# Kernel tuning notes

Hardware: AMD Instinct MI355X
Metric: run time of the kernel (lower is better)

## Reference

```python
import jax, jax.numpy as jnp
import numpy as np

N = 100000
INPLANES = 256
WIDTH = 104          # floor(256 * 26 / 64)
SCALE = 4
NUMS = SCALE - 1     # 3 branch convs
K = 27               # 3^3 kernel offsets for 3D kernel_size=3
EPS = 1e-5


def setup_inputs() -> dict:
    key = jax.random.key(0)
    ks = jax.random.split(key, 12)
    x_feat = jax.random.normal(ks[0], (N, INPLANES), dtype=jnp.float32)
    # neighbor map: index N means "no neighbor" (padded zero row)
    nbr_idx = jax.random.randint(ks[1], (N, K), 0, N + 1)
    ws = WIDTH * SCALE
    W1 = jax.random.normal(ks[2], (INPLANES, ws), dtype=jnp.float32) * (1.0 / np.sqrt(INPLANES))
    g1 = jnp.ones((ws,), jnp.float32)
    b1 = jnp.zeros((ws,), jnp.float32)
    Wc = jax.random.normal(ks[3], (NUMS, K, WIDTH, WIDTH), dtype=jnp.float32) * (1.0 / np.sqrt(K * WIDTH))
    gc = jnp.ones((NUMS, WIDTH), jnp.float32)
    bc = jnp.zeros((NUMS, WIDTH), jnp.float32)
    W3 = jax.random.normal(ks[4], (ws, INPLANES), dtype=jnp.float32) * (1.0 / np.sqrt(ws))
    g3 = jnp.ones((INPLANES,), jnp.float32)
    b3 = jnp.zeros((INPLANES,), jnp.float32)
    return {"x_feat": x_feat, "nbr_idx": nbr_idx, "W1": W1, "g1": g1, "b1": b1,
            "Wc": Wc, "gc": gc, "bc": bc, "W3": W3, "g3": g3, "b3": b3}


def _bn(x, g, b):
    # training-mode batch norm over the point dimension
    m = jnp.mean(x, axis=0)
    v = jnp.var(x, axis=0)
    return (x - m) * jax.lax.rsqrt(v + EPS) * g + b


def _sparse_conv(feat, nbr_idx, Wk):
    # gather-GEMM-scatter sparse conv: out[n] = sum_k feat[nbr[n,k]] @ Wk[k]
    # index == N hits the appended zero row (missing neighbor)
    fp = jnp.concatenate([feat, jnp.zeros((1, feat.shape[1]), feat.dtype)], axis=0)
    out = jnp.zeros((feat.shape[0], Wk.shape[2]), feat.dtype)
    for k in range(Wk.shape[0]):  # fixed small set of 27 kernel offsets
        out = out + fp[nbr_idx[:, k]] @ Wk[k]
    return out


def reference(x_feat, nbr_idx, W1, g1, b1, Wc, gc, bc, W3, g3, b3):
    out = jax.nn.relu(_bn(x_feat @ W1, g1, b1))          # [N, width*scale]
    spx = [out[:, i * WIDTH:(i + 1) * WIDTH] for i in range(SCALE)]
    parts = []
    sp = None
    for i in range(NUMS):
        # stype='normal', same coord map -> features_at_coordinates is identity
        sp_in = spx[i] if i == 0 else sp + spx[i]
        sp = jax.nn.relu(_bn(_sparse_conv(sp_in, nbr_idx, Wc[i]), gc[i], bc[i]))
        parts.append(sp)
    parts.append(spx[SCALE - 1])                          # scale != 1, normal
    cat = jnp.concatenate(parts, axis=1)                  # [N, width*scale]
    out = _bn(cat @ W3, g3, b3) + x_feat                  # residual (no downsample)
    return jax.nn.relu(out)
```

## Files before the change

kernel.cpp:

```cpp
#include <hip/hip_runtime.h>

#define NPTS 100000
#define INC 256
#define WID 104
#define WSC 416
#define KOFF 27
#define EPSV 1e-5f

typedef unsigned short u16;
typedef float f32x4 __attribute__((ext_vector_type(4)));
typedef short s16x8 __attribute__((ext_vector_type(8)));

__device__ __forceinline__ u16 f2bf(float f) {
  unsigned u = __builtin_bit_cast(unsigned, f);
  u += 0x7FFFu + ((u >> 16) & 1u);
  return (u16)(u >> 16);
}
__device__ __forceinline__ float bf2f(u16 h) {
  unsigned u = ((unsigned)h) << 16;
  return __builtin_bit_cast(float, u);
}
__device__ __forceinline__ void mfma16(f32x4& d, s16x8 a, s16x8 b) {
  asm("v_mfma_f32_16x16x32_bf16 %0, %1, %2, %0" : "+v"(d) : "v"(a), "v"(b));
}
__device__ __forceinline__ void rawbar() {
  __builtin_amdgcn_s_barrier();
  __builtin_amdgcn_sched_barrier(0);
}

#define ST1_OFF 0
#define STC_OFF 6656
#define STC_SZ 1664
#define ST3_OFF 11648
#define ST_TOTAL 15744

#define SPAD 128

__global__ __launch_bounds__(256) void k_prep_w1w3(const float* __restrict__ w1,
    const float* __restrict__ w3, u16* __restrict__ w1t, u16* __restrict__ w3t) {
  int i = blockIdx.x * 256 + threadIdx.x;
  if (i < 416 * 256) {
    int n = i >> 8, k = i & 255;
    w1t[i] = f2bf(w1[(size_t)k * WSC + n]);
  } else if (i < 2 * 416 * 256) {
    int o = i - 416 * 256;
    int n = o / WSC, k = o - n * WSC;
    w3t[o] = f2bf(w3[(size_t)k * INC + n]);
  }
}

__global__ __launch_bounds__(256) void k_prep_wc(const float* __restrict__ wc,
                                                 u16* __restrict__ wct) {
  __shared__ float w[WID * WID];
  int b = blockIdx.x, t = threadIdx.x;
  const float* s = wc + (size_t)b * WID * WID;
  for (int i = t; i < WID * WID; i += 256) w[i] = s[i];
  __syncthreads();
  u16* d = wct + (size_t)b * 112 * WID;
  for (int o = t; o < 112 * WID; o += 256) {
    int n = o / WID, kin = o - n * WID;
    d[o] = f2bf((n < WID) ? w[kin * WID + n] : 0.f);
  }
}

__global__ void k_init(float* __restrict__ st, u16* __restrict__ spxp) {
  const s16x8 hz = {0, 0, 0, 0, 0, 0, 0, 0};
  int i = blockIdx.x * 256 + threadIdx.x;
  if (i < ST_TOTAL) st[i] = 0.f;
  for (int task = i; task < (NPTS + 1) * 3; task += gridDim.x * 256) {
    int r = task / 3, c = task - 3 * r;
    *(s16x8*)(spxp + (size_t)r * SPAD + (13 + c) * 8) = hz;
  }
  if (blockIdx.x == 0 && threadIdx.x < 13)
    *(s16x8*)(spxp + (size_t)NPTS * SPAD + threadIdx.x * 8) = hz;
}

__global__ __launch_bounds__(256) void k_xbf(const float* __restrict__ x,
                                             u16* __restrict__ xb) {
  const int total = NPTS * INC / 8;
  for (int i = blockIdx.x * 256 + threadIdx.x; i < total; i += gridDim.x * 256) {
    const f32x4* s = (const f32x4*)(x + (size_t)i * 8);
    f32x4 v0 = s[0], v1 = s[1];
    s16x8 h;
#pragma unroll
    for (int j = 0; j < 4; ++j) { h[j] = (short)f2bf(v0[j]); h[4 + j] = (short)f2bf(v1[j]); }
    *(s16x8*)(xb + (size_t)i * 8) = h;
  }
}

__global__ __launch_bounds__(256) void k_gemm1(const u16* __restrict__ xb,
    const u16* __restrict__ w1t, u16* __restrict__ ys, float* __restrict__ stats) {
  const int n = blockIdx.x, xcd = n & 7, sgrp = n >> 3;
  const int cb = sgrp & 3, q = sgrp >> 2;
  const int rowbase = (xcd + 8 * q) * 128;
  if (rowbase >= NPTS) return;
  __shared__ char Al[128 * 128];
  __shared__ char Bl[112 * 128];
  const int t = threadIdx.x;
  const int lane = t & 63, wv = t >> 6, lr = lane & 15, lg = lane >> 4;
  const f32x4 fz = {0.f, 0.f, 0.f, 0.f};
  const s16x8 hz = {0, 0, 0, 0, 0, 0, 0, 0};
  f32x4 acc[2][7];
#pragma unroll
  for (int i = 0; i < 2; ++i)
#pragma unroll
    for (int j = 0; j < 7; ++j) acc[i][j] = fz;
  s16x8 pa[4], pb[4];

  auto issue = [&](int st) {
#pragma unroll
    for (int it = 0; it < 4; ++it) {
      int task = t + it * 256, r = task >> 3, c = task & 7, gr = rowbase + r;
      pa[it] = hz;
      if (gr < NPTS) pa[it] = *(const s16x8*)(xb + (size_t)gr * INC + st * 64 + c * 8);
      pb[it] = hz;
      if (task < 832)
        pb[it] = *(const s16x8*)(w1t + (size_t)(cb * WID + r) * INC + st * 64 + c * 8);
    }
  };
  auto writeT = [&]() {
#pragma unroll
    for (int it = 0; it < 4; ++it) {
      int task = t + it * 256, r = task >> 3, c = task & 7;
      *(s16x8*)(Al + ((r * 128 + c * 16) ^ ((r & 7) << 4))) = pa[it];
      if (task < 896) *(s16x8*)(Bl + ((r * 128 + c * 16) ^ ((r & 7) << 4))) = pb[it];
    }
  };
  auto compute = [&]() {
#pragma unroll
    for (int kc = 0; kc < 2; ++kc) {
      int co = kc * 64 + lg * 16;
      s16x8 a[2], b[7];
#pragma unroll
      for (int mt = 0; mt < 2; ++mt) {
        int r = wv * 32 + mt * 16 + lr;
        a[mt] = *(const s16x8*)(Al + ((r * 128 + co) ^ ((r & 7) << 4)));
      }
#pragma unroll
      for (int ct = 0; ct < 7; ++ct) {
        int r = ct * 16 + lr;
        b[ct] = *(const s16x8*)(Bl + ((r * 128 + co) ^ ((r & 7) << 4)));
      }
#pragma unroll
      for (int mt = 0; mt < 2; ++mt)
#pragma unroll
        for (int ct = 0; ct < 7; ++ct) mfma16(acc[mt][ct], a[mt], b[ct]);
    }
  };

  issue(0);
  for (int st = 0; st < 4; ++st) {
    writeT();
    __syncthreads();
    if (st < 3) issue(st + 1);
    compute();
    if (st < 3) rawbar();
  }
  __syncthreads();
  float* S = (float*)Al;
#pragma unroll
  for (int ct = 0; ct < 7; ++ct) {
    float s = 0.f, qq = 0.f;
#pragma unroll
    for (int mt = 0; mt < 2; ++mt)
#pragma unroll
      for (int j = 0; j < 4; ++j) { float v = acc[mt][ct][j]; s += v; qq += v * v; }
    s += __shfl_xor(s, 16); s += __shfl_xor(s, 32);
    qq += __shfl_xor(qq, 16); qq += __shfl_xor(qq, 32);
    if (lane < 16) {
      S[wv * 224 + ct * 16 + lane] = s;
      S[wv * 224 + 112 + ct * 16 + lane] = qq;
    }
  }
  __syncthreads();
  if (t < 224) {
    float v = S[t] + S[224 + t] + S[448 + t] + S[672 + t];
    int cl = (t < 112) ? t : t - 112;
    if (cl < WID) {
      float* base = stats + (sgrp & 7) * 832;
      atomicAdd(base + ((t < 112) ? 0 : WSC) + cb * WID + cl, v);
    }
  }
  __syncthreads();
#pragma unroll
  for (int mt = 0; mt < 2; ++mt)
#pragma unroll
    for (int ct = 0; ct < 7; ++ct)
#pragma unroll
      for (int j = 0; j < 4; ++j) {
        int r = rowbase + wv * 32 + mt * 16 + lg * 4 + j;
        int cl = ct * 16 + lr;
        if (r < NPTS && cl < WID)
          ys[((size_t)cb * NPTS + r) * WID + cl] = f2bf(acc[mt][ct][j]);
      }
}

__global__ __launch_bounds__(256) void k_conv(const u16* __restrict__ src,
    const int* __restrict__ nbr, const u16* __restrict__ wct,
    u16* __restrict__ z, float* __restrict__ stats) {
  __shared__ char Bl[112 * 208 + 64];
  const int t = threadIdx.x, rowbase = blockIdx.x * 128;
  const int lane = t & 63, wv = t >> 6, lr = lane & 15, lg = lane >> 4;
  const f32x4 fz = {0.f, 0.f, 0.f, 0.f};
  f32x4 acc[2][7];
#pragma unroll
  for (int i = 0; i < 2; ++i)
#pragma unroll
    for (int j = 0; j < 7; ++j) acc[i][j] = fz;
  s16x8 pa[2][4], pb[6];

  const int rm0 = rowbase + wv * 32 + lr, rm1 = rm0 + 16;
  const bool ok0 = rm0 < NPTS, ok1 = rm1 < NPTS;
  const int* np0 = nbr + (size_t)(ok0 ? rm0 : 0) * KOFF;
  const int* np1 = nbr + (size_t)(ok1 ? rm1 : 0) * KOFF;
  int in0, in1;

  auto loadB = [&](int k) {
#pragma unroll
    for (int it = 0; it < 6; ++it) {
      int task = t + it * 256;
      if (task < 1456) {
        int r = task / 13, c = task - 13 * r;
        pb[it] = *(const s16x8*)(wct + ((size_t)k * 112 + r) * WID + c * 8);
      }
    }
  };
  auto writeB = [&]() {
#pragma unroll
    for (int it = 0; it < 6; ++it) {
      int task = t + it * 256;
      if (task < 1456) {
        int r = task / 13, c = task - 13 * r;
        *(s16x8*)(Bl + r * 208 + c * 16) = pb[it];
      }
    }
  };

  {
    int i0 = ok0 ? np0[0] : NPTS, i1 = ok1 ? np1[0] : NPTS;
#pragma unroll
    for (int kc = 0; kc < 4; ++kc) {
      pa[0][kc] = *(const s16x8*)(src + (size_t)i0 * SPAD + kc * 32 + lg * 8);
      pa[1][kc] = *(const s16x8*)(src + (size_t)i1 * SPAD + kc * 32 + lg * 8);
    }
    loadB(0);
    in0 = ok0 ? np0[1] : NPTS;
    in1 = ok1 ? np1[1] : NPTS;
  }

  for (int k = 0; k < KOFF; ++k) {
    writeB();
    __syncthreads();
    if (k < KOFF - 1) loadB(k + 1);
    const bool more = k < KOFF - 1;
#pragma unroll
    for (int kc = 0; kc < 4; ++kc) {
      s16x8 bf[7];
#pragma unroll
      for (int ct = 0; ct < 7; ++ct)
        bf[ct] = *(const s16x8*)(Bl + (ct * 16 + lr) * 208 + kc * 64 + lg * 16);
#pragma unroll
      for (int ct = 0; ct < 7; ++ct) {
        mfma16(acc[0][ct], pa[0][kc], bf[ct]);
        mfma16(acc[1][ct], pa[1][kc], bf[ct]);
      }
      if (more) {
        pa[0][kc] = *(const s16x8*)(src + (size_t)in0 * SPAD + kc * 32 + lg * 8);
        pa[1][kc] = *(const s16x8*)(src + (size_t)in1 * SPAD + kc * 32 + lg * 8);
      }
    }
    if (k < KOFF - 2) {
      in0 = ok0 ? np0[k + 2] : NPTS;
      in1 = ok1 ? np1[k + 2] : NPTS;
    }
    rawbar();
  }

  __syncthreads();
  float* S = (float*)Bl;
#pragma unroll
  for (int ct = 0; ct < 7; ++ct) {
    float s = 0.f, qq = 0.f;
#pragma unroll
    for (int mt = 0; mt < 2; ++mt)
#pragma unroll
      for (int j = 0; j < 4; ++j) { float v = acc[mt][ct][j]; s += v; qq += v * v; }
    s += __shfl_xor(s, 16); s += __shfl_xor(s, 32);
    qq += __shfl_xor(qq, 16); qq += __shfl_xor(qq, 32);
    if (lane < 16) {
      S[wv * 224 + ct * 16 + lane] = s;
      S[wv * 224 + 112 + ct * 16 + lane] = qq;
    }
  }
  __syncthreads();
  if (t < 224) {
    float v = S[t] + S[224 + t] + S[448 + t] + S[672 + t];
    int cl = (t < 112) ? t : t - 112;
    if (cl < WID) {
      float* base = stats + (blockIdx.x & 7) * 208;
      atomicAdd(base + ((t < 112) ? 0 : WID) + cl, v);
    }
  }
#pragma unroll
  for (int mt = 0; mt < 2; ++mt)
#pragma unroll
    for (int ct = 0; ct < 7; ++ct)
#pragma unroll
      for (int j = 0; j < 4; ++j) {
        int r = rowbase + wv * 32 + mt * 16 + lg * 4 + j;
        int cl = ct * 16 + lr;
        if (r < NPTS && cl < WID)
          z[(size_t)r * WID + cl] = f2bf(acc[mt][ct][j]);
      }
}

__global__ __launch_bounds__(256) void k_gemm3(const u16* __restrict__ z0,
    const u16* __restrict__ z1, const u16* __restrict__ z2, const u16* __restrict__ ys,
    const u16* __restrict__ w3t, const float* __restrict__ ST,
    const float* __restrict__ gcp, const float* __restrict__ bcp,
    const float* __restrict__ g1, const float* __restrict__ b1,
    u16* __restrict__ ob, float* __restrict__ st3) {
  const int n = blockIdx.x, xcd = n & 7, sgrp = n >> 3;
  const int cb = sgrp & 1, q = sgrp >> 1;
  const int rowbase = (xcd + 8 * q) * 128;
  if (rowbase >= NPTS) return;
  __shared__ char Al[128 * 128];
  __shared__ char Bl[128 * 128];
  __shared__ float sscl[416], ssft[416];
  const int t = threadIdx.x;
  const int lane = t & 63, wv = t >> 6, lr = lane & 15, lg = lane >> 4;
  const int wr = wv >> 1, wc = wv & 1;
  const f32x4 fz = {0.f, 0.f, 0.f, 0.f};
  const s16x8 hz = {0, 0, 0, 0, 0, 0, 0, 0};
  const u16* ys3 = ys + (size_t)3 * NPTS * WID;
  for (int i = t; i < 416; i += 256) {
    float s = 0.f, qq = 0.f, gg, bb;
    if (i < 312) {
      int p = i / 104, c = i - p * 104;
      const float* base = ST + STC_OFF + p * STC_SZ;
#pragma unroll
      for (int bk = 0; bk < 8; ++bk) { s += base[bk * 208 + c]; qq += base[bk * 208 + 104 + c]; }
      gg = gcp[i]; bb = bcp[i];
    } else {
#pragma unroll
      for (int bk = 0; bk < 8; ++bk) { s += ST[bk * 832 + i]; qq += ST[bk * 832 + 416 + i]; }
      gg = g1[i]; bb = b1[i];
    }
    float m = s * (1.f / NPTS);
    float var = qq * (1.f / NPTS) - m * m;
    float rs = rsqrtf(var + EPSV);
    float sc = rs * gg;
    sscl[i] = sc; ssft[i] = bb - m * sc;
  }
  f32x4 acc[4][4];
#pragma unroll
  for (int i = 0; i < 4; ++i)
#pragma unroll
    for (int j = 0; j < 4; ++j) acc[i][j] = fz;
  s16x8 pa[4], pb[4];

  auto issue = [&](int st) {
#pragma unroll
    for (int it = 0; it < 4; ++it) {
      int task = t + it * 256, r = task >> 3, c = task & 7;
      int gr = rowbase + r, gq = st * 8 + c;
      pa[it] = hz;
      if (gr < NPTS && gq < 52) {
        int p = gq / 13, cc8 = (gq - p * 13) * 8;
        const u16* s = (p == 0) ? z0 + (size_t)gr * WID + cc8
                     : (p == 1) ? z1 + (size_t)gr * WID + cc8
                     : (p == 2) ? z2 + (size_t)gr * WID + cc8
                                : ys3 + (size_t)gr * WID + cc8;
        pa[it] = *(const s16x8*)s;
      }
      int gk = st * 64 + c * 8;
      pb[it] = hz;
      if (gk < WSC) pb[it] = *(const s16x8*)(w3t + (size_t)(cb * 128 + r) * WSC + gk);
    }
  };
  auto writeT = [&](int st) {
#pragma unroll
    for (int it = 0; it < 4; ++it) {
      int task = t + it * 256, r = task >> 3, c = task & 7;
      int gr = rowbase + r, gq = st * 8 + c;
      s16x8 h = hz;
      if (gr < NPTS && gq < 52) {
        int p = gq / 13;
        int colb = p * WID + (gq - p * 13) * 8;
#pragma unroll
        for (int j = 0; j < 8; ++j) {
          float f = fmaxf(bf2f((u16)pa[it][j]) * sscl[colb + j] + ssft[colb + j], 0.f);
          h[j] = (short)f2bf(f);
        }
      }
      *(s16x8*)(Al + ((r * 128 + c * 16) ^ ((r & 7) << 4))) = h;
      *(s16x8*)(Bl + ((r * 128 + c * 16) ^ ((r & 7) << 4))) = pb[it];
    }
  };
  auto compute = [&]() {
#pragma unroll
    for (int kc = 0; kc < 2; ++kc) {
      int co = kc * 64 + lg * 16;
      s16x8 a[4], b[4];
#pragma unroll
      for (int mt = 0; mt < 4; ++mt) {
        int r = wr * 64 + mt * 16 + lr;
        a[mt] = *(const s16x8*)(Al + ((r * 128 + co) ^ ((r & 7) << 4)));
      }
#pragma unroll
      for (int ct = 0; ct < 4; ++ct) {
        int r = wc * 64 + ct * 16 + lr;
        b[ct] = *(const s16x8*)(Bl + ((r * 128 + co) ^ ((r & 7) << 4)));
      }
#pragma unroll
      for (int mt = 0; mt < 4; ++mt)
#pragma unroll
        for (int ct = 0; ct < 4; ++ct) mfma16(acc[mt][ct], a[mt], b[ct]);
    }
  };

  issue(0);
  __syncthreads();
  for (int st = 0; st < 7; ++st) {
    writeT(st);
    __syncthreads();
    if (st < 6) issue(st + 1);
    compute();
    if (st < 6) rawbar();
  }
  __syncthreads();
  float* S = (float*)Al;
#pragma unroll
  for (int ct = 0; ct < 4; ++ct) {
    float s = 0.f, qq = 0.f;
#pragma unroll
    for (int mt = 0; mt < 4; ++mt)
#pragma unroll
      for (int j = 0; j < 4; ++j) { float v = acc[mt][ct][j]; s += v; qq += v * v; }
    s += __shfl_xor(s, 16); s += __shfl_xor(s, 32);
    qq += __shfl_xor(qq, 16); qq += __shfl_xor(qq, 32);
    if (lane < 16) {
      S[wv * 128 + ct * 16 + lane] = s;
      S[wv * 128 + 64 + ct * 16 + lane] = qq;
    }
  }
  __syncthreads();
  {
    float* base = st3 + (sgrp & 7) * 512;
    if (t < 64) atomicAdd(base + cb * 128 + t, S[t] + S[256 + t]);
    else if (t < 128) atomicAdd(base + INC + cb * 128 + (t - 64), S[64 + t - 64] + S[320 + t - 64]);
    else if (t < 192) atomicAdd(base + cb * 128 + 64 + (t - 128), S[128 + t - 128] + S[384 + t - 128]);
    else atomicAdd(base + INC + cb * 128 + 64 + (t - 192), S[192 + t - 192] + S[448 + t - 192]);
  }
#pragma unroll
  for (int mt = 0; mt < 4; ++mt)
#pragma unroll
    for (int ct = 0; ct < 4; ++ct)
#pragma unroll
      for (int j = 0; j < 4; ++j) {
        int r = rowbase + wr * 64 + mt * 16 + lg * 4 + j;
        int col = cb * 128 + wc * 64 + ct * 16 + lr;
        if (r < NPTS) ob[(size_t)r * INC + col] = f2bf(acc[mt][ct][j]);
      }
}

template <int HASZ>
__global__ __launch_bounds__(256) void k_mix(const u16* __restrict__ ys, int slab,
    const float* __restrict__ ST, int yoff,
    const float* __restrict__ g1, const float* __restrict__ b1,
    const u16* __restrict__ z, const float* __restrict__ stc,
    const float* __restrict__ gcb, const float* __restrict__ bcb,
    u16* __restrict__ spx) {
  __shared__ float s1c[104], f1c[104], szc[104], fzc[104];
  const int t = threadIdx.x;
  if (t < 104) {
    float s = 0.f, q = 0.f;
#pragma unroll
    for (int bk = 0; bk < 8; ++bk) { s += ST[bk * 832 + yoff + t]; q += ST[bk * 832 + 416 + yoff + t]; }
    float m = s * (1.f / NPTS);
    float var = q * (1.f / NPTS) - m * m;
    float rs = rsqrtf(var + EPSV);
    float sc = rs * g1[yoff + t];
    s1c[t] = sc; f1c[t] = b1[yoff + t] - m * sc;
  } else if (HASZ && t >= 128 && t < 232) {
    int c = t - 128;
    float s = 0.f, q = 0.f;
#pragma unroll
    for (int bk = 0; bk < 8; ++bk) { s += stc[bk * 208 + c]; q += stc[bk * 208 + 104 + c]; }
    float m = s * (1.f / NPTS);
    float var = q * (1.f / NPTS) - m * m;
    float rs = rsqrtf(var + EPSV);
    float sc = rs * gcb[c];
    szc[c] = sc; fzc[c] = bcb[c] - m * sc;
  }
  __syncthreads();
  const u16* yb = ys + (size_t)slab * NPTS * WID;
  const int total = NPTS * 13;
  for (int i = blockIdx.x * 256 + t; i < total; i += gridDim.x * 256) {
    int r = i / 13, cc = i - r * 13;
    s16x8 y = *(const s16x8*)(yb + (size_t)r * WID + cc * 8);
    s16x8 zv;
    if (HASZ) zv = *(const s16x8*)(z + (size_t)r * WID + cc * 8);
    s16x8 o;
#pragma unroll
    for (int j = 0; j < 8; ++j) {
      int c = cc * 8 + j;
      float f = fmaxf(bf2f((u16)y[j]) * s1c[c] + f1c[c], 0.f);
      if (HASZ) f += fmaxf(bf2f((u16)zv[j]) * szc[c] + fzc[c], 0.f);
      o[j] = (short)f2bf(f);
    }
    *(s16x8*)(spx + (size_t)r * SPAD + cc * 8) = o;
  }
}

__global__ __launch_bounds__(256) void k_final(const u16* __restrict__ ob,
    const u16* __restrict__ xb, const float* __restrict__ ST3,
    const float* __restrict__ g3, const float* __restrict__ b3,
    float* __restrict__ out) {
  __shared__ float sc3[256], sf3[256];
  const int t = threadIdx.x;
  {
    float s = 0.f, q = 0.f;
#pragma unroll
    for (int bk = 0; bk < 8; ++bk) { s += ST3[bk * 512 + t]; q += ST3[bk * 512 + 256 + t]; }
    float m = s * (1.f / NPTS);
    float var = q * (1.f / NPTS) - m * m;
    float rs = rsqrtf(var + EPSV);
    float sc = rs * g3[t];
    sc3[t] = sc; sf3[t] = b3[t] - m * sc;
  }
  __syncthreads();
  const int total = NPTS * 32;
  for (int i = blockIdx.x * 256 + t; i < total; i += gridDim.x * 256) {
    int r = i >> 5, cc = i & 31;
    s16x8 o = *(const s16x8*)(ob + (size_t)r * INC + cc * 8);
    s16x8 xv = *(const s16x8*)(xb + (size_t)r * INC + cc * 8);
    f32x4 v0, v1;
#pragma unroll
    for (int j = 0; j < 4; ++j) {
      int c = cc * 8 + j;
      v0[j] = fmaxf(bf2f((u16)o[j]) * sc3[c] + sf3[c] + bf2f((u16)xv[j]), 0.f);
    }
#pragma unroll
    for (int j = 0; j < 4; ++j) {
      int c = cc * 8 + 4 + j;
      v1[j] = fmaxf(bf2f((u16)o[4 + j]) * sc3[c] + sf3[c] + bf2f((u16)xv[4 + j]), 0.f);
    }
    f32x4* dp = (f32x4*)(out + (size_t)r * INC + cc * 8);
    dp[0] = v0; dp[1] = v1;
  }
}

extern "C" void kernel_launch(void* const* d_in, const int* in_sizes, int n_in,
                              void* d_out, int out_size, void* d_ws, size_t ws_size,
                              hipStream_t stream) {
  const float* x  = (const float*)d_in[0];
  const int* nbr  = (const int*)d_in[1];
  const float* W1 = (const float*)d_in[2];
  const float* g1 = (const float*)d_in[3];
  const float* b1 = (const float*)d_in[4];
  const float* Wc = (const float*)d_in[5];
  const float* gc = (const float*)d_in[6];
  const float* bc = (const float*)d_in[7];
  const float* W3 = (const float*)d_in[8];
  const float* g3 = (const float*)d_in[9];
  const float* b3 = (const float*)d_in[10];
  float* out = (float*)d_out;

  char* ws = (char*)d_ws;
  size_t off = 0;
  auto alloc = [&](size_t nbytes) {
    char* p = ws + off;
    off += (nbytes + 255) & ~(size_t)255;
    return p;
  };
  u16* W1T = (u16*)alloc(416 * 256 * 2);
  u16* W3T = (u16*)alloc(256 * 416 * 2);
  u16* WCT = (u16*)alloc((size_t)3 * 27 * 112 * 104 * 2);
  u16* XB  = (u16*)alloc((size_t)NPTS * INC * 2);
  u16* Y1S = (u16*)alloc((size_t)4 * NPTS * WID * 2);
  u16* Z0  = (u16*)alloc((size_t)NPTS * WID * 2);
  u16* Z1  = (u16*)alloc((size_t)NPTS * WID * 2);
  u16* Z2  = (u16*)alloc((size_t)NPTS * WID * 2);
  u16* OB  = (u16*)alloc((size_t)NPTS * INC * 2);
  u16* SPX = (u16*)alloc((size_t)(NPTS + 1) * SPAD * 2);
  float* ST = (float*)alloc(ST_TOTAL * 4);
  float* ST1  = ST + ST1_OFF;
  float* STC0 = ST + STC_OFF;
  float* STC1 = ST + STC_OFF + STC_SZ;
  float* STC2 = ST + STC_OFF + 2 * STC_SZ;
  float* ST3  = ST + ST3_OFF;

  k_prep_w1w3<<<832, 256, 0, stream>>>(W1, W3, W1T, W3T);
  k_prep_wc<<<81, 256, 0, stream>>>(Wc, WCT);
  k_init<<<256, 256, 0, stream>>>(ST, SPX);
  k_xbf<<<2048, 256, 0, stream>>>(x, XB);

  k_gemm1<<<3136, 256, 0, stream>>>(XB, W1T, Y1S, ST1);

  const size_t WCL = (size_t)27 * 112 * WID;
  k_mix<0><<<2048, 256, 0, stream>>>(Y1S, 0, ST1, 0, g1, b1,
                                     nullptr, nullptr, nullptr, nullptr, SPX);
  k_conv<<<782, 256, 0, stream>>>(SPX, nbr, WCT, Z0, STC0);
  k_mix<1><<<2048, 256, 0, stream>>>(Y1S, 1, ST1, 104, g1, b1,
                                     Z0, STC0, gc, bc, SPX);
  k_conv<<<782, 256, 0, stream>>>(SPX, nbr, WCT + WCL, Z1, STC1);
  k_mix<1><<<2048, 256, 0, stream>>>(Y1S, 2, ST1, 208, g1, b1,
                                     Z1, STC1, gc + 104, bc + 104, SPX);
  k_conv<<<782, 256, 0, stream>>>(SPX, nbr, WCT + 2 * WCL, Z2, STC2);

  k_gemm3<<<1568, 256, 0, stream>>>(Z0, Z1, Z2, Y1S, W3T, ST, gc, bc, g1, b1, OB, ST3);
  k_final<<<2048, 256, 0, stream>>>(OB, XB, ST3, g3, b3, out);
}
```

Baseline: 710.4 us.

## Fuse branch mix into sparse conv via grid-wide barrier and merge prep kernels

The BN+ReLU+add mix that builds the next branch input now runs at the tail of each conv kernel. A software grid barrier (atomic counter with spin-wait) waits until every block has finished the conv and published its stats. After that, each block mixes its own 128 rows while its z output is likely still in cache. The three weight-prep and init kernels are merged into one launch, and the conv gets a 4-blocks-per-CU occupancy bound. This removes launch gaps and a separate pass over z, but it relies on all 782 blocks being co-resident and adds spin-wait cost.

```diff
diff --git a/kernel.cpp b/kernel.cpp
--- a/kernel.cpp
+++ b/kernel.cpp
@@ -6,6 +6,7 @@
 #define WSC 416
 #define KOFF 27
 #define EPSV 1e-5f
+#define NCONVBLK 782
 
 typedef unsigned short u16;
 typedef float f32x4 __attribute__((ext_vector_type(4)));
@@ -32,47 +33,49 @@
 #define STC_OFF 6656
 #define STC_SZ 1664
 #define ST3_OFF 11648
-#define ST_TOTAL 15744
+#define BAR_OFF 15744
+#define ST_TOTAL 15752
 
 #define SPAD 128
 
-__global__ __launch_bounds__(256) void k_prep_w1w3(const float* __restrict__ w1,
-    const float* __restrict__ w3, u16* __restrict__ w1t, u16* __restrict__ w3t) {
-  int i = blockIdx.x * 256 + threadIdx.x;
-  if (i < 416 * 256) {
-    int n = i >> 8, k = i & 255;
-    w1t[i] = f2bf(w1[(size_t)k * WSC + n]);
-  } else if (i < 2 * 416 * 256) {
-    int o = i - 416 * 256;
-    int n = o / WSC, k = o - n * WSC;
-    w3t[o] = f2bf(w3[(size_t)k * INC + n]);
-  }
-}
-
-__global__ __launch_bounds__(256) void k_prep_wc(const float* __restrict__ wc,
-                                                 u16* __restrict__ wct) {
-  __shared__ float w[WID * WID];
-  int b = blockIdx.x, t = threadIdx.x;
-  const float* s = wc + (size_t)b * WID * WID;
-  for (int i = t; i < WID * WID; i += 256) w[i] = s[i];
-  __syncthreads();
-  u16* d = wct + (size_t)b * 112 * WID;
-  for (int o = t; o < 112 * WID; o += 256) {
-    int n = o / WID, kin = o - n * WID;
-    d[o] = f2bf((n < WID) ? w[kin * WID + n] : 0.f);
-  }
-}
-
-__global__ void k_init(float* __restrict__ st, u16* __restrict__ spxp) {
-  const s16x8 hz = {0, 0, 0, 0, 0, 0, 0, 0};
-  int i = blockIdx.x * 256 + threadIdx.x;
-  if (i < ST_TOTAL) st[i] = 0.f;
-  for (int task = i; task < (NPTS + 1) * 3; task += gridDim.x * 256) {
-    int r = task / 3, c = task - 3 * r;
-    *(s16x8*)(spxp + (size_t)r * SPAD + (13 + c) * 8) = hz;
-  }
-  if (blockIdx.x == 0 && threadIdx.x < 13)
-    *(s16x8*)(spxp + (size_t)NPTS * SPAD + threadIdx.x * 8) = hz;
+__global__ __launch_bounds__(256) void k_prep(const float* __restrict__ w1,
+    const float* __restrict__ w3, const float* __restrict__ wc,
+    u16* __restrict__ w1t, u16* __restrict__ w3t, u16* __restrict__ wct,
+    float* __restrict__ st, u16* __restrict__ spxp) {
+  const int blk = blockIdx.x, t = threadIdx.x;
+  if (blk < 832) {
+    int i = blk * 256 + t;
+    if (i < 416 * 256) {
+      int n = i >> 8, k = i & 255;
+      w1t[i] = f2bf(w1[(size_t)k * WSC + n]);
+    } else {
+      int o = i - 416 * 256;
+      int n = o / WSC, k = o - n * WSC;
+      w3t[o] = f2bf(w3[(size_t)k * INC + n]);
+    }
+  } else if (blk < 913) {
+    __shared__ float w[WID * WID];
+    int b = blk - 832;
+    const float* s = wc + (size_t)b * WID * WID;
+    for (int i = t; i < WID * WID; i += 256) w[i] = s[i];
+    __syncthreads();
+    u16* d = wct + (size_t)b * 112 * WID;
+    for (int o = t; o < 112 * WID; o += 256) {
+      int n = o / WID, kin = o - n * WID;
+      d[o] = f2bf((n < WID) ? w[kin * WID + n] : 0.f);
+    }
+  } else {
+    const s16x8 hz = {0, 0, 0, 0, 0, 0, 0, 0};
+    int b2 = blk - 913;
+    int i = b2 * 256 + t;
+    if (i < ST_TOTAL) st[i] = 0.f;
+    for (int task = i; task < (NPTS + 1) * 3; task += 256 * 256) {
+      int r = task / 3, c = task - 3 * r;
+      *(s16x8*)(spxp + (size_t)r * SPAD + (13 + c) * 8) = hz;
+    }
+    if (b2 == 0 && t < 13)
+      *(s16x8*)(spxp + (size_t)NPTS * SPAD + t * 8) = hz;
+  }
 }
 
 __global__ __launch_bounds__(256) void k_xbf(const float* __restrict__ x,
@@ -195,9 +198,14 @@
       }
 }
 
-__global__ __launch_bounds__(256) void k_conv(const u16* __restrict__ src,
+template <int NEXT>
+__global__ __launch_bounds__(256, 4) void k_conv(const u16* __restrict__ src,
     const int* __restrict__ nbr, const u16* __restrict__ wct,
-    u16* __restrict__ z, float* __restrict__ stats) {
+    u16* __restrict__ z, float* __restrict__ stats,
+    const u16* __restrict__ ynext, const float* __restrict__ ST1, int yoff,
+    const float* __restrict__ g1, const float* __restrict__ b1,
+    const float* __restrict__ gcb, const float* __restrict__ bcb,
+    u16* __restrict__ spxout, int* __restrict__ barcnt) {
   __shared__ char Bl[112 * 208 + 64];
   const int t = threadIdx.x, rowbase = blockIdx.x * 128;
   const int lane = t & 63, wv = t >> 6, lr = lane & 15, lg = lane >> 4;
@@ -312,6 +320,59 @@
         if (r < NPTS && cl < WID)
           z[(size_t)r * WID + cl] = f2bf(acc[mt][ct][j]);
       }
+
+  if (NEXT) {
+    __syncthreads();
+    if (t == 0) {
+      __threadfence();
+      atomicAdd(barcnt, 1);
+      while (__hip_atomic_load(barcnt, __ATOMIC_ACQUIRE, __HIP_MEMORY_SCOPE_AGENT) < NCONVBLK) {
+        __builtin_amdgcn_s_sleep(8);
+      }
+    }
+    __syncthreads();
+    float* s1c = (float*)Bl;
+    float* f1c = s1c + 104;
+    float* szc = f1c + 104;
+    float* fzc = szc + 104;
+    if (t < 104) {
+      float s = 0.f, q = 0.f;
+#pragma unroll
+      for (int bk = 0; bk < 8; ++bk) { s += ST1[bk * 832 + yoff + t]; q += ST1[bk * 832 + 416 + yoff + t]; }
+      float m = s * (1.f / NPTS);
+      float var = q * (1.f / NPTS) - m * m;
+      float rs = rsqrtf(var + EPSV);
+      float sc = rs * g1[yoff + t];
+      s1c[t] = sc; f1c[t] = b1[yoff + t] - m * sc;
+    } else if (t >= 128 && t < 232) {
+      int c = t - 128;
+      float s = 0.f, q = 0.f;
+#pragma unroll
+      for (int bk = 0; bk < 8; ++bk) { s += stats[bk * 208 + c]; q += stats[bk * 208 + 104 + c]; }
+      float m = s * (1.f / NPTS);
+      float var = q * (1.f / NPTS) - m * m;
+      float rs = rsqrtf(var + EPSV);
+      float sc = rs * gcb[c];
+      szc[c] = sc; fzc[c] = bcb[c] - m * sc;
+    }
+    __syncthreads();
+    for (int task = t; task < 128 * 13; task += 256) {
+      int rr = task / 13, cc = task - 13 * rr;
+      int r = rowbase + rr;
+      if (r >= NPTS) break;
+      s16x8 zv = *(const s16x8*)(z + (size_t)r * WID + cc * 8);
+      s16x8 yv = *(const s16x8*)(ynext + (size_t)r * WID + cc * 8);
+      s16x8 o;
+#pragma unroll
+      for (int j = 0; j < 8; ++j) {
+        int c = cc * 8 + j;
+        float f = fmaxf(bf2f((u16)yv[j]) * s1c[c] + f1c[c], 0.f)
+                + fmaxf(bf2f((u16)zv[j]) * szc[c] + fzc[c], 0.f);
+        o[j] = (short)f2bf(f);
+      }
+      *(s16x8*)(spxout + (size_t)r * SPAD + cc * 8) = o;
+    }
+  }
 }
 
 __global__ __launch_bounds__(256) void k_gemm3(const u16* __restrict__ z0,
@@ -464,50 +525,31 @@
       }
 }
 
-template <int HASZ>
-__global__ __launch_bounds__(256) void k_mix(const u16* __restrict__ ys, int slab,
-    const float* __restrict__ ST, int yoff,
-    const float* __restrict__ g1, const float* __restrict__ b1,
-    const u16* __restrict__ z, const float* __restrict__ stc,
-    const float* __restrict__ gcb, const float* __restrict__ bcb,
+__global__ __launch_bounds__(256) void k_mix0(const u16* __restrict__ ys,
+    const float* __restrict__ ST, const float* __restrict__ g1, const float* __restrict__ b1,
     u16* __restrict__ spx) {
-  __shared__ float s1c[104], f1c[104], szc[104], fzc[104];
+  __shared__ float s1c[104], f1c[104];
   const int t = threadIdx.x;
   if (t < 104) {
     float s = 0.f, q = 0.f;
 #pragma unroll
-    for (int bk = 0; bk < 8; ++bk) { s += ST[bk * 832 + yoff + t]; q += ST[bk * 832 + 416 + yoff + t]; }
+    for (int bk = 0; bk < 8; ++bk) { s += ST[bk * 832 + t]; q += ST[bk * 832 + 416 + t]; }
     float m = s * (1.f / NPTS);
     float var = q * (1.f / NPTS) - m * m;
     float rs = rsqrtf(var + EPSV);
-    float sc = rs * g1[yoff + t];
-    s1c[t] = sc; f1c[t] = b1[yoff + t] - m * sc;
-  } else if (HASZ && t >= 128 && t < 232) {
-    int c = t - 128;
-    float s = 0.f, q = 0.f;
-#pragma unroll
-    for (int bk = 0; bk < 8; ++bk) { s += stc[bk * 208 + c]; q += stc[bk * 208 + 104 + c]; }
-    float m = s * (1.f / NPTS);
-    float var = q * (1.f / NPTS) - m * m;
-    float rs = rsqrtf(var + EPSV);
-    float sc = rs * gcb[c];
-    szc[c] = sc; fzc[c] = bcb[c] - m * sc;
-  }
-  __syncthreads();
-  const u16* yb = ys + (size_t)slab * NPTS * WID;
+    float sc = rs * g1[t];
+    s1c[t] = sc; f1c[t] = b1[t] - m * sc;
+  }
+  __syncthreads();
   const int total = NPTS * 13;
   for (int i = blockIdx.x * 256 + t; i < total; i += gridDim.x * 256) {
     int r = i / 13, cc = i - r * 13;
-    s16x8 y = *(const s16x8*)(yb + (size_t)r * WID + cc * 8);
-    s16x8 zv;
-    if (HASZ) zv = *(const s16x8*)(z + (size_t)r * WID + cc * 8);
+    s16x8 y = *(const s16x8*)(ys + (size_t)r * WID + cc * 8);
     s16x8 o;
 #pragma unroll
     for (int j = 0; j < 8; ++j) {
       int c = cc * 8 + j;
-      float f = fmaxf(bf2f((u16)y[j]) * s1c[c] + f1c[c], 0.f);
-      if (HASZ) f += fmaxf(bf2f((u16)zv[j]) * szc[c] + fzc[c], 0.f);
-      o[j] = (short)f2bf(f);
+      o[j] = (short)f2bf(fmaxf(bf2f((u16)y[j]) * s1c[c] + f1c[c], 0.f));
     }
     *(s16x8*)(spx + (size_t)r * SPAD + cc * 8) = o;
   }
@@ -590,24 +632,23 @@
   float* STC1 = ST + STC_OFF + STC_SZ;
   float* STC2 = ST + STC_OFF + 2 * STC_SZ;
   float* ST3  = ST + ST3_OFF;
-
-  k_prep_w1w3<<<832, 256, 0, stream>>>(W1, W3, W1T, W3T);
-  k_prep_wc<<<81, 256, 0, stream>>>(Wc, WCT);
-  k_init<<<256, 256, 0, stream>>>(ST, SPX);
+  int* BAR = (int*)(ST + BAR_OFF);
+
+  k_prep<<<1169, 256, 0, stream>>>(W1, W3, Wc, W1T, W3T, WCT, ST, SPX);
   k_xbf<<<2048, 256, 0, stream>>>(x, XB);
 
   k_gemm1<<<3136, 256, 0, stream>>>(XB, W1T, Y1S, ST1);
+  k_mix0<<<2048, 256, 0, stream>>>(Y1S, ST1, g1, b1, SPX);
 
   const size_t WCL = (size_t)27 * 112 * WID;
-  k_mix<0><<<2048, 256, 0, stream>>>(Y1S, 0, ST1, 0, g1, b1,
-                                     nullptr, nullptr, nullptr, nullptr, SPX);
-  k_conv<<<782, 256, 0, stream>>>(SPX, nbr, WCT, Z0, STC0);
-  k_mix<1><<<2048, 256, 0, stream>>>(Y1S, 1, ST1, 104, g1, b1,
-                                     Z0, STC0, gc, bc, SPX);
-  k_conv<<<782, 256, 0, stream>>>(SPX, nbr, WCT + WCL, Z1, STC1);
-  k_mix<1><<<2048, 256, 0, stream>>>(Y1S, 2, ST1, 208, g1, b1,
-                                     Z1, STC1, gc + 104, bc + 104, SPX);
-  k_conv<<<782, 256, 0, stream>>>(SPX, nbr, WCT + 2 * WCL, Z2, STC2);
+  const u16* YS1 = Y1S + (size_t)1 * NPTS * WID;
+  const u16* YS2 = Y1S + (size_t)2 * NPTS * WID;
+  k_conv<1><<<NCONVBLK, 256, 0, stream>>>(SPX, nbr, WCT, Z0, STC0,
+      YS1, ST1, 104, g1, b1, gc, bc, SPX, BAR);
+  k_conv<1><<<NCONVBLK, 256, 0, stream>>>(SPX, nbr, WCT + WCL, Z1, STC1,
+      YS2, ST1, 208, g1, b1, gc + 104, bc + 104, SPX, BAR + 1);
+  k_conv<0><<<NCONVBLK, 256, 0, stream>>>(SPX, nbr, WCT + 2 * WCL, Z2, STC2,
+      nullptr, nullptr, 0, nullptr, nullptr, nullptr, nullptr, nullptr, nullptr);
 
   k_gemm3<<<1568, 256, 0, stream>>>(Z0, Z1, Z2, Y1S, W3T, ST, gc, bc, g1, b1, OB, ST3);
   k_final<<<2048, 256, 0, stream>>>(OB, XB, ST3, g3, b3, out);
```

Result: slower. 2.119 ms (+198.3%).
